# Kernel optimization log

Measured on AMD Instinct MI355X. Metric: run time of the kernel, lower is better.

The kernel has to match this reference:

```python
import jax, jax.numpy as jnp
import numpy as np

NUM_CLASSES = 22
H_IMG, W_IMG = 256, 320
VOTE_STEPS = 160          # number of discrete steps each pixel votes along its ray
VOTE_THRESH = 0.5         # inlier threshold used by HoughVoterPyTorch


def setup_inputs() -> dict:
    key = jax.random.key(0)
    ks = jax.random.split(key, 24)
    B = 4
    rn = lambda k, s, sc=1.0: (jax.random.normal(k, s, jnp.float32) * sc)
    inp = {
        'x1': rn(ks[0], (B, 512, 8, 10)),
        'x2': rn(ks[1], (B, 256, 16, 20)),
        'x3': rn(ks[2], (B, 128, 32, 40)),
        'x4': rn(ks[3], (B, 64, 64, 80)),
        'x5': rn(ks[4], (B, 64, 128, 160)),
        'depth': jax.random.uniform(ks[5], (B, 1, H_IMG, W_IMG), jnp.float32, 0.5, 3.0),
    }
    raw = jax.random.uniform(ks[6], (B, NUM_CLASSES, H_IMG, W_IMG), jnp.float32)
    inp['seg'] = jnp.where(raw > 0.97, raw, 0.0)  # sparse per-class responses
    inp['fx'] = jnp.float32(572.4); inp['fy'] = jnp.float32(573.6)
    inp['px'] = jnp.float32(W_IMG / 2); inp['py'] = jnp.float32(H_IMG / 2)
    # ConvTranspose2d weights in torch layout [Cin, Cout, kH, kW]
    inp['w5'] = rn(ks[7], (512, 256, 4, 4), 0.02); inp['b5'] = jnp.zeros((256,), jnp.float32)
    inp['w4'] = rn(ks[8], (512, 128, 4, 4), 0.02); inp['b4'] = jnp.zeros((128,), jnp.float32)
    inp['w3'] = rn(ks[9], (256, 64, 4, 4), 0.03);  inp['b3'] = jnp.zeros((64,), jnp.float32)
    inp['w2'] = rn(ks[10], (128, 64, 4, 4), 0.04); inp['b2'] = jnp.zeros((64,), jnp.float32)
    inp['w1'] = rn(ks[11], (128, 64, 4, 4), 0.04); inp['b1'] = jnp.zeros((64,), jnp.float32)
    inp['wv'] = rn(ks[12], (3 * NUM_CLASSES, 64), 0.1); inp['bv'] = jnp.zeros((3 * NUM_CLASSES,), jnp.float32)
    inp['wc'] = rn(ks[13], (NUM_CLASSES, 64), 0.1);     inp['bc'] = jnp.zeros((NUM_CLASSES,), jnp.float32)
    return inp


def conv_t(x, w, b):
    # torch ConvTranspose2d(k=4, s=2, p=1) == dilated conv with flipped kernel
    k = jnp.flip(w, (2, 3)).transpose(1, 0, 2, 3)  # [Cout, Cin, 4, 4]
    y = jax.lax.conv_general_dilated(x, k, (1, 1), ((2, 2), (2, 2)),
                                     lhs_dilation=(2, 2),
                                     dimension_numbers=('NCHW', 'OIHW', 'NCHW'))
    return y + b[None, :, None, None]


def hough_vote(seg2d, dirs, depth2d, fx, fy, px, py):
    # seg2d: [H,W] fused fg prob; dirs: [H,W,2] (dx,dy); depth2d: [H,W]
    H, W = seg2d.shape
    n = dirs / (jnp.linalg.norm(dirs, axis=-1, keepdims=True) + 1e-6)
    u = n[..., 0].reshape(-1)
    v = n[..., 1].reshape(-1)
    ys, xs = jnp.meshgrid(jnp.arange(H, dtype=jnp.float32),
                          jnp.arange(W, dtype=jnp.float32), indexing='ij')
    xs = xs.reshape(-1); ys = ys.reshape(-1)
    w = (seg2d * (seg2d > VOTE_THRESH)).reshape(-1)  # weighted fg votes

    def step(acc, t):
        xt = jnp.round(xs + t * u).astype(jnp.int32)
        yt = jnp.round(ys + t * v).astype(jnp.int32)
        inb = (xt >= 0) & (xt < W) & (yt >= 0) & (yt < H)
        idx = jnp.clip(yt, 0, H - 1) * W + jnp.clip(xt, 0, W - 1)
        return acc.at[idx].add(jnp.where(inb, w, 0.0)), None

    acc, _ = jax.lax.scan(step, jnp.zeros(H * W, jnp.float32),
                          jnp.arange(1, VOTE_STEPS + 1, dtype=jnp.float32))
    vote_map = acc.reshape(H, W)
    ci = jnp.argmax(acc)
    cy = (ci // W).astype(jnp.float32)
    cx = (ci % W).astype(jnp.float32)
    mask = (seg2d > VOTE_THRESH).astype(jnp.float32)
    tz = jnp.sum(depth2d * mask) / (jnp.sum(mask) + 1e-6)
    tx = (cx - px) * tz / fx
    ty = (cy - py) * tz / fy
    return vote_map, jnp.stack([cx, cy]), jnp.stack([tx, ty, tz])


def reference(x1, x2, x3, x4, x5, depth, seg, fx, fy, px, py,
              w5, b5, w4, b4, w3, b3, w2, b2, w1, b1, wv, bv, wc, bc):
    x = jax.nn.relu(conv_t(x1, w5, b5))
    x = jax.nn.relu(conv_t(jnp.concatenate([x, x2], 1), w4, b4))
    x = jax.nn.relu(conv_t(jnp.concatenate([x, x3], 1), w3, b3))
    x = jax.nn.relu(conv_t(jnp.concatenate([x, x4], 1), w2, b2))
    x = jax.nn.relu(conv_t(jnp.concatenate([x, x5], 1), w1, b1))
    bottom_vertex = jnp.einsum('bchw,oc->bohw', x, wv) + bv[None, :, None, None]
    logits = jnp.einsum('bchw,oc->bohw', x, wc) + bc[None, :, None, None]
    bottom_label = jnp.argmax(logits, axis=1)
    center_dirs = jnp.transpose(bottom_vertex[:, :2], (0, 2, 3, 1))  # [B,H,W,2]
    seg_fused = jnp.clip(jnp.sum(seg, axis=1), 0.0, 1.0)             # [B,H,W]
    vote_maps, centers, translations = jax.vmap(
        hough_vote, in_axes=(0, 0, 0, None, None, None, None)
    )(seg_fused, center_dirs, depth[:, 0], fx, fy, px, py)
    return bottom_vertex, bottom_label, vote_maps, centers, translations
```

## Files before the change

kernel.cpp:

```cpp
#include <hip/hip_runtime.h>
#include <cstdint>
#include <cstddef>

#define H_IMG 256
#define W_IMG 320
#define HW_IMG (H_IMG * W_IMG)
#define NCLS 22
#define VOTE_STEPS 160
#define TW 64
#define TH 64
#define NTX 5
#define NTY 4
#define NTILE (NTX * NTY)
#define NCHUNK 16
#define CHPIX (HW_IMG / NCHUNK)

__global__ void repack_kernel(const float* __restrict__ w, double* __restrict__ wp,
                              int CIN, int COUT) {
    int total = CIN * COUT * 16;
    for (int i = blockIdx.x * blockDim.x + threadIdx.x; i < total;
         i += gridDim.x * blockDim.x) {
        int j = i & 3;
        int co = (i >> 2) % COUT;
        int rest = (i >> 2) / COUT;
        int cin = rest % CIN;
        int pp = rest / CIN;
        int ry = pp >> 1, rx = pp & 1;
        int dy = j >> 1, dx = j & 1;
        int ky = 3 - ry - 2 * dy;
        int kx = 3 - rx - 2 * dx;
        wp[i] = (double)w[((size_t)cin * COUT + co) * 16 + ky * 4 + kx];
    }
}

__global__ void repackR_kernel(const float* __restrict__ w, double* __restrict__ wr,
                               int CIN, int COUT) {
    int NCOG = COUT >> 4;
    int total = CIN * COUT * 16;
    for (int i = blockIdx.x * blockDim.x + threadIdx.x; i < total;
         i += gridDim.x * blockDim.x) {
        int tap = i & 3;
        int co = (i >> 2) & 15;
        int rest = i >> 6;
        int cin = rest % CIN;
        int pc = rest / CIN;
        int cog = pc % NCOG;
        int pp = pc / NCOG;
        int ry = pp >> 1, rx = pp & 1;
        int dy = tap >> 1, dxx = tap & 1;
        int ky = 3 - ry - 2 * dy;
        int kx = 3 - rx - 2 * dxx;
        wr[i] = (double)w[((size_t)cin * COUT + (cog * 16 + co)) * 16 + ky * 4 + kx];
    }
}

__global__ void transpose_d_kernel(const float* __restrict__ w, double* __restrict__ wt,
                                   int O, int K) {
    int i = blockIdx.x * blockDim.x + threadIdx.x;
    if (i < O * K) {
        int o = i / K, k = i - o * K;
        wt[k * O + o] = (double)w[i];
    }
}

template <bool RELU_A, bool ADBL>
__global__ __launch_bounds__(320) void convt_part_kernel(
    const void* __restrict__ inA_, int CA,
    const float* __restrict__ inB, int CB,
    const double* __restrict__ wp,
    double* __restrict__ parts,
    int COUT, int Hin, int Win, int nSplit, int B, int TOT) {
    const int NCO = 16;
    const int CIN = CA + CB;
    const int cog = blockIdx.y >> 2;
    const int pp = blockIdx.y & 3;
    const int ry = pp >> 1, rx = pp & 1;
    const int b = blockIdx.z % B;
    const int sp = blockIdx.z / B;
    const int cinPer = CIN / nSplit;
    const int c0 = sp * cinPer, c1 = c0 + cinPer;
    const int co0 = cog * NCO;
    const int plane = Hin * Win;
    const int Hout = Hin * 2, Wout = Win * 2;
    const int bs = blockDim.x;
    double* out = parts + (size_t)sp * TOT;

    __shared__ double wl[64 * 64];
    for (int i = threadIdx.x; i < cinPer * 64; i += bs) {
        int ci = i >> 6, k = i & 63;
        wl[i] = wp[(((size_t)pp * CIN + c0 + ci) * COUT + co0) * 4 + k];
    }
    __syncthreads();

    for (int p = blockIdx.x * bs + threadIdx.x; p < plane; p += gridDim.x * bs) {
        int m = p / Win, n = p - m * Win;
        int iy0 = m + ry - 1, ix0 = n + rx - 1;
        int oy = 2 * m + ry, ox = 2 * n + rx;
        double f00 = (iy0 >= 0 && ix0 >= 0) ? 1.0 : 0.0;
        double f01 = (iy0 >= 0 && ix0 + 1 < Win) ? 1.0 : 0.0;
        double f10 = (iy0 + 1 < Hin && ix0 >= 0) ? 1.0 : 0.0;
        double f11 = (iy0 + 1 < Hin && ix0 + 1 < Win) ? 1.0 : 0.0;
        int cy0 = max(iy0, 0), cy1 = min(iy0 + 1, Hin - 1);
        int cx0 = max(ix0, 0), cx1 = min(ix0 + 1, Win - 1);
        int o00 = cy0 * Win + cx0, o01 = cy0 * Win + cx1;
        int o10 = cy1 * Win + cx0, o11 = cy1 * Win + cx1;

        double acc[16];
#pragma unroll
        for (int k = 0; k < 16; ++k) acc[k] = 0.0;

        int a0 = min(c0, CA), a1 = min(c1, CA);
        for (int c = a0; c < a1; ++c) {
            double x00, x01, x10, x11;
            if (ADBL) {
                const double* s = (const double*)inA_ + ((size_t)b * CA + c) * plane;
                x00 = f00 * s[o00]; x01 = f01 * s[o01];
                x10 = f10 * s[o10]; x11 = f11 * s[o11];
            } else {
                const float* s = (const float*)inA_ + ((size_t)b * CA + c) * plane;
                x00 = f00 * (double)s[o00]; x01 = f01 * (double)s[o01];
                x10 = f10 * (double)s[o10]; x11 = f11 * (double)s[o11];
            }
            if (RELU_A) {
                x00 = fmax(x00, 0.0); x01 = fmax(x01, 0.0);
                x10 = fmax(x10, 0.0); x11 = fmax(x11, 0.0);
            }
            const double2* w2 = (const double2*)&wl[(c - c0) * 64];
#pragma unroll
            for (int k = 0; k < 16; ++k) {
                double2 wa = w2[k * 2], wb = w2[k * 2 + 1];
                acc[k] += x00 * wa.x + x01 * wa.y + x10 * wb.x + x11 * wb.y;
            }
        }
        if (CB > 0 && c1 > CA) {
            int b0 = max(c0, CA) - CA, b1 = c1 - CA;
            const float* srcB = inB + (size_t)b * CB * plane;
            for (int c = b0; c < b1; ++c) {
                const float* s = srcB + (size_t)c * plane;
                double x00 = f00 * (double)s[o00], x01 = f01 * (double)s[o01];
                double x10 = f10 * (double)s[o10], x11 = f11 * (double)s[o11];
                const double2* w2 = (const double2*)&wl[(c + CA - c0) * 64];
#pragma unroll
                for (int k = 0; k < 16; ++k) {
                    double2 wa = w2[k * 2], wb = w2[k * 2 + 1];
                    acc[k] += x00 * wa.x + x01 * wa.y + x10 * wb.x + x11 * wb.y;
                }
            }
        }

        size_t ob = ((size_t)b * COUT + co0) * (size_t)Hout * Wout +
                    (size_t)oy * Wout + ox;
#pragma unroll
        for (int k = 0; k < 16; ++k)
            out[ob + (size_t)k * Hout * Wout] = acc[k];
    }
}

__global__ __launch_bounds__(320) void convt_part_l1_kernel(
    const float* __restrict__ xin, int CIN,
    const double* __restrict__ wp,
    double* __restrict__ parts,
    int COUT, int nSplit, int B, int TOT) {
    const int Hin = 8, Win = 10, plane = 80;
    const int Hout = 16, Wout = 20;
    const int cog = blockIdx.y;
    const int b = blockIdx.z % B;
    const int sp = blockIdx.z / B;
    const int cinPer = CIN / nSplit;
    const int c0 = sp * cinPer;
    const int co0 = cog * 16;
    const int pp = threadIdx.x / plane;
    const int p = threadIdx.x - pp * plane;
    const int ry = pp >> 1, rx = pp & 1;
    double* out = parts + (size_t)sp * TOT;

    __shared__ double wl[4 * 32 * 64];
    for (int i = threadIdx.x; i < 4 * cinPer * 64; i += 320) {
        int k = i & 63;
        int ci = (i >> 6) % cinPer;
        int pq = (i >> 6) / cinPer;
        wl[i] = wp[(((size_t)pq * CIN + c0 + ci) * COUT + co0) * 4 + k];
    }
    __syncthreads();

    int m = p / Win, n = p - m * Win;
    int iy0 = m + ry - 1, ix0 = n + rx - 1;
    int oy = 2 * m + ry, ox = 2 * n + rx;
    double f00 = (iy0 >= 0 && ix0 >= 0) ? 1.0 : 0.0;
    double f01 = (iy0 >= 0 && ix0 + 1 < Win) ? 1.0 : 0.0;
    double f10 = (iy0 + 1 < Hin && ix0 >= 0) ? 1.0 : 0.0;
    double f11 = (iy0 + 1 < Hin && ix0 + 1 < Win) ? 1.0 : 0.0;
    int cy0 = max(iy0, 0), cy1 = min(iy0 + 1, Hin - 1);
    int cx0 = max(ix0, 0), cx1 = min(ix0 + 1, Win - 1);
    int o00 = cy0 * Win + cx0, o01 = cy0 * Win + cx1;
    int o10 = cy1 * Win + cx0, o11 = cy1 * Win + cx1;

    double acc[16];
#pragma unroll
    for (int k = 0; k < 16; ++k) acc[k] = 0.0;

    const float* s = xin + ((size_t)b * CIN + c0) * plane;
    const double* wpp = &wl[pp * cinPer * 64];
    for (int c = 0; c < cinPer; ++c) {
        double x00 = f00 * (double)s[o00], x01 = f01 * (double)s[o01];
        double x10 = f10 * (double)s[o10], x11 = f11 * (double)s[o11];
        const double2* w2 = (const double2*)&wpp[c * 64];
#pragma unroll
        for (int k = 0; k < 16; ++k) {
            double2 wa = w2[k * 2], wb = w2[k * 2 + 1];
            acc[k] += x00 * wa.x + x01 * wa.y + x10 * wb.x + x11 * wb.y;
        }
        s += plane;
    }

    size_t ob = ((size_t)b * COUT + co0) * (size_t)Hout * Wout +
                (size_t)oy * Wout + ox;
#pragma unroll
    for (int k = 0; k < 16; ++k)
        out[ob + (size_t)k * Hout * Wout] = acc[k];
}

__global__ void reduce_part_kernel(const double* __restrict__ parts,
                                   const float* __restrict__ bias,
                                   double* __restrict__ out,
                                   int nSplit, int COUT, int HWo, int TOT) {
    int i = blockIdx.x * blockDim.x + threadIdx.x;
    if (i < TOT) {
        double a = (double)bias[(i / HWo) % COUT];
        for (int sp = 0; sp < nSplit; ++sp) a += parts[(size_t)sp * TOT + i];
        out[i] = a;
    }
}

template <int PX>
__global__ __launch_bounds__(256) void convt_reg_kernel(
    const double* __restrict__ zin, const float* __restrict__ xin,
    const double* __restrict__ wr,
    const float* __restrict__ bias,
    double* __restrict__ out,
    int COUT, int Hin, int Win) {
    const int NCOG = COUT >> 4;
    const int plane = Hin * Win;
    const int Wq = Win / PX;
    const int cog = blockIdx.y >> 2, pp = blockIdx.y & 3;
    const int ry = pp >> 1, rx = pp & 1;
    const int b = blockIdx.z;
    __shared__ double wl[4096];

    int t = blockIdx.x * 256 + threadIdx.x;
    int m = t / Wq, n0 = (t - m * Wq) * PX;
    int r0 = m + ry - 1, r1 = r0 + 1;
    double mr0 = (r0 >= 0) ? 1.0 : 0.0;
    double mr1 = (r1 < Hin) ? 1.0 : 0.0;
    int cr0 = max(r0, 0) * Win, cr1 = min(r1, Hin - 1) * Win;
    const int ib = rx ? 0 : 1;
    const int eidx = rx ? PX : 0;
    int eoff = rx ? min(n0 + PX, Win - 1) : max(n0 - 1, 0);
    double me = rx ? ((n0 + PX < Win) ? 1.0 : 0.0) : ((n0 > 0) ? 1.0 : 0.0);
    double me0 = me * mr0, me1 = me * mr1;

    double acc[16][PX];
#pragma unroll
    for (int k = 0; k < 16; ++k) {
        double bvv = (double)bias[cog * 16 + k];
#pragma unroll
        for (int tt = 0; tt < PX; ++tt) acc[k][tt] = bvv;
    }

    const double* wbase = wr + (size_t)(pp * NCOG + cog) * 128 * 64;

    for (int i = threadIdx.x; i < 4096; i += 256) wl[i] = wbase[i];
    __syncthreads();
    {
        const double* s = zin + (size_t)b * 64 * plane;
        for (int c = 0; c < 64; ++c) {
            double xa0[PX + 1], xa1[PX + 1];
#pragma unroll
            for (int j = 0; j < PX / 2; ++j) {
                double2 v0 = *(const double2*)(s + cr0 + n0 + 2 * j);
                double2 v1 = *(const double2*)(s + cr1 + n0 + 2 * j);
                xa0[ib + 2 * j] = mr0 * fmax(v0.x, 0.0);
                xa0[ib + 2 * j + 1] = mr0 * fmax(v0.y, 0.0);
                xa1[ib + 2 * j] = mr1 * fmax(v1.x, 0.0);
                xa1[ib + 2 * j + 1] = mr1 * fmax(v1.y, 0.0);
            }
            xa0[eidx] = me0 * fmax(s[cr0 + eoff], 0.0);
            xa1[eidx] = me1 * fmax(s[cr1 + eoff], 0.0);
            const double2* w2 = (const double2*)&wl[c * 64];
#pragma unroll
            for (int co = 0; co < 16; ++co) {
                double2 wa = w2[co * 2], wb = w2[co * 2 + 1];
#pragma unroll
                for (int tt = 0; tt < PX; ++tt)
                    acc[co][tt] += wa.x * xa0[tt] + wa.y * xa0[tt + 1] +
                                   wb.x * xa1[tt] + wb.y * xa1[tt + 1];
            }
            s += plane;
        }
    }
    __syncthreads();
    for (int i = threadIdx.x; i < 4096; i += 256) wl[i] = wbase[4096 + i];
    __syncthreads();
    {
        const float* s = xin + (size_t)b * 64 * plane;
        for (int c = 0; c < 64; ++c) {
            double xa0[PX + 1], xa1[PX + 1];
#pragma unroll
            for (int j = 0; j < PX / 2; ++j) {
                float2 v0 = *(const float2*)(s + cr0 + n0 + 2 * j);
                float2 v1 = *(const float2*)(s + cr1 + n0 + 2 * j);
                xa0[ib + 2 * j] = mr0 * (double)v0.x;
                xa0[ib + 2 * j + 1] = mr0 * (double)v0.y;
                xa1[ib + 2 * j] = mr1 * (double)v1.x;
                xa1[ib + 2 * j + 1] = mr1 * (double)v1.y;
            }
            xa0[eidx] = me0 * (double)s[cr0 + eoff];
            xa1[eidx] = me1 * (double)s[cr1 + eoff];
            const double2* w2 = (const double2*)&wl[c * 64];
#pragma unroll
            for (int co = 0; co < 16; ++co) {
                double2 wa = w2[co * 2], wb = w2[co * 2 + 1];
#pragma unroll
                for (int tt = 0; tt < PX; ++tt)
                    acc[co][tt] += wa.x * xa0[tt] + wa.y * xa0[tt + 1] +
                                   wb.x * xa1[tt] + wb.y * xa1[tt + 1];
            }
            s += plane;
        }
    }

    int oy = 2 * m + ry;
    size_t ob = (size_t)(b * COUT + cog * 16) * plane * 4 + (size_t)oy * (Win * 2);
#pragma unroll
    for (int co = 0; co < 16; ++co)
#pragma unroll
        for (int tt = 0; tt < PX; ++tt)
            out[ob + (size_t)co * plane * 4 + 2 * (n0 + tt) + rx] = acc[co][tt];
}

__global__ __launch_bounds__(256) void head_lds_kernel(
    const double* __restrict__ z5,
    const double* __restrict__ wvT,
    const float* __restrict__ bv,
    const double* __restrict__ wcT,
    const float* __restrict__ bc,
    float* __restrict__ vert, double* __restrict__ dirs,
    float* __restrict__ label) {
    int p = blockIdx.x * 256 + threadIdx.x;
    int half = blockIdx.y;
    int b = blockIdx.z;
    __shared__ double wl[64 * 44];
    if (half == 0) {
        for (int i = threadIdx.x; i < 64 * 44; i += 256) {
            int c = i / 44, k = i - c * 44;
            wl[i] = wvT[c * 66 + k];
        }
    } else {
        for (int i = threadIdx.x; i < 64 * 44; i += 256) {
            int c = i / 44, k = i - c * 44;
            wl[i] = (k < 22) ? wvT[c * 66 + 44 + k] : wcT[c * 22 + (k - 22)];
        }
    }
    __syncthreads();

    const double* xp = z5 + (size_t)b * 64 * HW_IMG + p;
    if (half == 0) {
        double acc[44];
#pragma unroll
        for (int k = 0; k < 44; ++k) acc[k] = (double)bv[k];
        for (int c = 0; c < 64; ++c) {
            double x = fmax(xp[(size_t)c * HW_IMG], 0.0);
            const double2* w2 = (const double2*)&wl[c * 44];
#pragma unroll
            for (int j = 0; j < 22; ++j) {
                double2 w = w2[j];
                acc[2 * j] += x * w.x; acc[2 * j + 1] += x * w.y;
            }
        }
        float* op = vert + (size_t)b * 66 * HW_IMG + p;
#pragma unroll
        for (int k = 0; k < 44; ++k) op[(size_t)k * HW_IMG] = (float)acc[k];
        dirs[(size_t)b * 2 * HW_IMG + p] = acc[0];
        dirs[(size_t)b * 2 * HW_IMG + HW_IMG + p] = acc[1];
    } else {
        double acc[22], lg[22];
#pragma unroll
        for (int k = 0; k < 22; ++k) { acc[k] = (double)bv[44 + k]; lg[k] = (double)bc[k]; }
        for (int c = 0; c < 64; ++c) {
            double x = fmax(xp[(size_t)c * HW_IMG], 0.0);
            const double2* w2 = (const double2*)&wl[c * 44];
#pragma unroll
            for (int j = 0; j < 11; ++j) {
                double2 w = w2[j];
                acc[2 * j] += x * w.x; acc[2 * j + 1] += x * w.y;
            }
#pragma unroll
            for (int j = 0; j < 11; ++j) {
                double2 w = w2[11 + j];
                lg[2 * j] += x * w.x; lg[2 * j + 1] += x * w.y;
            }
        }
        float* op = vert + ((size_t)b * 66 + 44) * HW_IMG + p;
#pragma unroll
        for (int k = 0; k < 22; ++k) op[(size_t)k * HW_IMG] = (float)acc[k];
        int bi = 0; double bvv = lg[0];
#pragma unroll
        for (int k = 1; k < 22; ++k)
            if (lg[k] > bvv) { bvv = lg[k]; bi = k; }
        label[(size_t)b * HW_IMG + p] = (float)bi;
    }
}

__global__ __launch_bounds__(256) void vote_prep_kernel(
    const float* __restrict__ seg, const float* __restrict__ depth,
    const double* __restrict__ dirs,
    double* __restrict__ rayS, double* __restrict__ rayU,
    double* __restrict__ rayV, double* __restrict__ rayRU,
    double* __restrict__ rayRV, double* __restrict__ rayN,
    double* __restrict__ sums) {
    int p = blockIdx.x * 256 + threadIdx.x;
    int b = blockIdx.z;
    double s = 0.0;
    const float* sp = seg + (size_t)b * NCLS * HW_IMG + p;
    for (int c = 0; c < NCLS; ++c) s += (double)sp[(size_t)c * HW_IMG];
    s = fmin(fmax(s, 0.0), 1.0);
    bool msk = s > 0.5;
    double d = (double)depth[(size_t)b * HW_IMG + p];
    double dm = msk ? d : 0.0;
    double mm = msk ? 1.0 : 0.0;
    for (int off = 32; off > 0; off >>= 1) {
        dm += __shfl_down(dm, off);
        mm += __shfl_down(mm, off);
    }
    __shared__ double sdm[4], smm[4];
    int wid = threadIdx.x >> 6, lane = threadIdx.x & 63;
    if (lane == 0) { sdm[wid] = dm; smm[wid] = mm; }
    __syncthreads();
    if (threadIdx.x == 0) {
        atomicAdd(&sums[b * 2 + 0], sdm[0] + sdm[1] + sdm[2] + sdm[3]);
        atomicAdd(&sums[b * 2 + 1], smm[0] + smm[1] + smm[2] + smm[3]);
    }
    size_t idx = (size_t)b * HW_IMG + p;
    if (msk) {
        double dx = dirs[(size_t)b * 2 * HW_IMG + p];
        double dy = dirs[(size_t)b * 2 * HW_IMG + HW_IMG + p];
        double nrm = sqrt(dx * dx + dy * dy) + 1e-6;
        double u = dx / nrm, v = dy / nrm;
        double xf = (double)(p % W_IMG), yf = (double)(p / W_IMG);
        double tmax = 1e30;
        if (u > 1e-9)       tmax = fmin(tmax, ((double)W_IMG - 0.25 - xf) / u);
        else if (u < -1e-9) tmax = fmin(tmax, (-0.75 - xf) / u);
        if (v > 1e-9)       tmax = fmin(tmax, ((double)H_IMG - 0.25 - yf) / v);
        else if (v < -1e-9) tmax = fmin(tmax, (-0.75 - yf) / v);
        int nst = VOTE_STEPS;
        if (tmax < (double)VOTE_STEPS) nst = (int)tmax + 1;
        rayS[idx] = s;
        rayU[idx] = u;
        rayV[idx] = v;
        rayRU[idx] = (u != 0.0) ? 1.0 / u : 0.0;
        rayRV[idx] = (v != 0.0) ? 1.0 / v : 0.0;
        rayN[idx] = (double)nst;
    } else {
        rayS[idx] = 0.0;
    }
}

__global__ __launch_bounds__(256) void vote_tile_kernel(
    const double* __restrict__ rayS, const double* __restrict__ rayU,
    const double* __restrict__ rayV, const double* __restrict__ rayRU,
    const double* __restrict__ rayRV, const double* __restrict__ rayN,
    double* __restrict__ vparts) {
    int chunk = blockIdx.x;
    int tile = blockIdx.y;
    int b = blockIdx.z;
    int tx0 = (tile % NTX) * TW, ty0 = (tile / NTX) * TH;
    __shared__ double vt[TW * TH];
    for (int i = threadIdx.x; i < TW * TH; i += 256) vt[i] = 0.0;
    __syncthreads();

    size_t base = (size_t)b * HW_IMG;
    int p0 = chunk * CHPIX;
    for (int q = threadIdx.x; q < CHPIX; q += 256) {
        int p = p0 + q;
        double s = rayS[base + p];
        if (s == 0.0) continue;
        double u = rayU[base + p], v = rayV[base + p];
        double ru = rayRU[base + p], rv = rayRV[base + p];
        int nst = (int)rayN[base + p];
        double xf = (double)(p % W_IMG), yf = (double)(p / W_IMG);
        double ta = 1.0, tb = (double)nst;
        if (ru != 0.0) {
            double lo = ((double)(tx0 - 1) - xf) * ru;
            double hi = ((double)(tx0 + TW) - xf) * ru;
            ta = fmax(ta, fmin(lo, hi));
            tb = fmin(tb, fmax(lo, hi));
        } else {
            if (xf < (double)(tx0 - 1) || xf > (double)(tx0 + TW)) continue;
        }
        if (rv != 0.0) {
            double lo = ((double)(ty0 - 1) - yf) * rv;
            double hi = ((double)(ty0 + TH) - yf) * rv;
            ta = fmax(ta, fmin(lo, hi));
            tb = fmin(tb, fmax(lo, hi));
        } else {
            if (yf < (double)(ty0 - 1) || yf > (double)(ty0 + TH)) continue;
        }
        if (ta > tb) continue;
        int t0 = (int)ceil(ta), t1 = (int)floor(tb);
        for (int t = t0; t <= t1; ++t) {
            double tf = (double)t;
            int xi = (int)rint(xf + tf * u);
            int yi = (int)rint(yf + tf * v);
            if (xi >= tx0 && xi < tx0 + TW && yi >= ty0 && yi < ty0 + TH)
                atomicAdd(&vt[(yi - ty0) * TW + (xi - tx0)], s);
        }
    }
    __syncthreads();
    double* dst = vparts + (((size_t)chunk * 4 + b) * NTILE + tile) * (TW * TH);
    for (int i = threadIdx.x; i < TW * TH; i += 256) dst[i] = vt[i];
}

__global__ void vote_reduce_kernel(const double* __restrict__ vparts,
                                   double* __restrict__ voteacc,
                                   float* __restrict__ vote) {
    int i = blockIdx.x * 256 + threadIdx.x;
    if (i < 4 * HW_IMG) {
        int b = i / HW_IMG, cell = i - b * HW_IMG;
        int y = cell / W_IMG, x = cell - y * W_IMG;
        int tile = (y / TH) * NTX + (x / TW);
        int ci = (y % TH) * TW + (x % TW);
        double a = 0.0;
        for (int c = 0; c < NCHUNK; ++c)
            a += vparts[(((size_t)c * 4 + b) * NTILE + tile) * (TW * TH) + ci];
        voteacc[i] = a;
        vote[i] = (float)a;
    }
}

__global__ __launch_bounds__(1024) void center_d_kernel(
    const double* __restrict__ voteacc, const double* __restrict__ sums,
    const float* __restrict__ fx, const float* __restrict__ fy,
    const float* __restrict__ px, const float* __restrict__ py,
    float* __restrict__ centers, float* __restrict__ transl) {
    int b = blockIdx.x;
    const double* vb = voteacc + (size_t)b * HW_IMG;
    double best = -1.0;
    int bi = HW_IMG;
    for (int i = threadIdx.x; i < HW_IMG; i += 1024) {
        double v = vb[i];
        if (v > best || (v == best && i < bi)) { best = v; bi = i; }
    }
    for (int off = 32; off > 0; off >>= 1) {
        double ov = __shfl_down(best, off);
        int oi = __shfl_down(bi, off);
        if (ov > best || (ov == best && oi < bi)) { best = ov; bi = oi; }
    }
    __shared__ double sbv[16];
    __shared__ int sbi[16];
    int wid = threadIdx.x >> 6, lane = threadIdx.x & 63;
    if (lane == 0) { sbv[wid] = best; sbi[wid] = bi; }
    __syncthreads();
    if (threadIdx.x == 0) {
        for (int q = 1; q < 16; ++q)
            if (sbv[q] > best || (sbv[q] == best && sbi[q] < bi)) {
                best = sbv[q]; bi = sbi[q];
            }
        double cx = (double)(bi % W_IMG), cy = (double)(bi / W_IMG);
        double tz = sums[b * 2 + 0] / (sums[b * 2 + 1] + 1e-6);
        double tx = (cx - (double)px[0]) * tz / (double)fx[0];
        double ty = (cy - (double)py[0]) * tz / (double)fy[0];
        centers[b * 2 + 0] = (float)cx;
        centers[b * 2 + 1] = (float)cy;
        transl[b * 3 + 0] = (float)tx;
        transl[b * 3 + 1] = (float)ty;
        transl[b * 3 + 2] = (float)tz;
    }
}

extern "C" void kernel_launch(void* const* d_in, const int* in_sizes, int n_in,
                              void* d_out, int out_size, void* d_ws, size_t ws_size,
                              hipStream_t stream) {
    const float* x1 = (const float*)d_in[0];
    const float* x2 = (const float*)d_in[1];
    const float* x3 = (const float*)d_in[2];
    const float* x4 = (const float*)d_in[3];
    const float* x5 = (const float*)d_in[4];
    const float* depth = (const float*)d_in[5];
    const float* seg = (const float*)d_in[6];
    const float* fx = (const float*)d_in[7];
    const float* fy = (const float*)d_in[8];
    const float* px = (const float*)d_in[9];
    const float* py = (const float*)d_in[10];
    const float* w5 = (const float*)d_in[11];
    const float* b5 = (const float*)d_in[12];
    const float* w4 = (const float*)d_in[13];
    const float* b4 = (const float*)d_in[14];
    const float* w3 = (const float*)d_in[15];
    const float* b3 = (const float*)d_in[16];
    const float* w2 = (const float*)d_in[17];
    const float* b2 = (const float*)d_in[18];
    const float* w1 = (const float*)d_in[19];
    const float* b1 = (const float*)d_in[20];
    const float* wv = (const float*)d_in[21];
    const float* bv = (const float*)d_in[22];
    const float* wc = (const float*)d_in[23];
    const float* bc = (const float*)d_in[24];

    float* out = (float*)d_out;
    float* vert = out;
    float* label = vert + (size_t)4 * 66 * HW_IMG;
    float* vote = label + (size_t)4 * HW_IMG;
    float* centers = vote + (size_t)4 * HW_IMG;
    float* transl = centers + 8;

    double* zA = (double*)d_ws;
    double* zB = zA + 20971520;
    double* dirs = zB + 5242880;
    double* voteacc = dirs + 655360;
    double* sums = voteacc + 327680;
    double* wp5 = sums + 8;
    double* wp4 = wp5 + 2097152;
    double* wp3 = wp4 + 1048576;
    double* wr2 = wp3 + 262144;
    double* wr1 = wr2 + 131072;
    double* wvT = wr1 + 131072;
    double* wcT = wvT + 4224;
    double* z1 = zA; double* z2 = zB; double* z3 = zA; double* z4 = zB; double* z5 = zA;
    double* parts = zA + 2000000;
    double* rayS = zB;
    double* rayU = zB + 327680;
    double* rayV = zB + 2 * 327680;
    double* rayRU = zB + 3 * 327680;
    double* rayRV = zB + 4 * 327680;
    double* rayN = zB + 5 * 327680;
    double* vparts = zA;

    hipMemsetAsync(sums, 0, 8 * sizeof(double), stream);

    auto rp = [&](const float* w, double* wp, int CIN, int COUT) {
        int total = CIN * COUT * 16;
        repack_kernel<<<(total + 255) / 256, 256, 0, stream>>>(w, wp, CIN, COUT);
    };
    rp(w5, wp5, 512, 256);
    rp(w4, wp4, 512, 128);
    rp(w3, wp3, 256, 64);
    repackR_kernel<<<(131072 + 255) / 256, 256, 0, stream>>>(w2, wr2, 128, 64);
    repackR_kernel<<<(131072 + 255) / 256, 256, 0, stream>>>(w1, wr1, 128, 64);
    transpose_d_kernel<<<(66 * 64 + 255) / 256, 256, 0, stream>>>(wv, wvT, 66, 64);
    transpose_d_kernel<<<(22 * 64 + 255) / 256, 256, 0, stream>>>(wc, wcT, 22, 64);

    convt_part_l1_kernel<<<dim3(1, 16, 64), 320, 0, stream>>>(
        x1, 512, wp5, parts, 256, 16, 4, 327680);
    reduce_part_kernel<<<1280, 256, 0, stream>>>(parts, b5, z1, 16, 256, 320, 327680);
    convt_part_kernel<true, true><<<dim3(1, 32, 32), 320, 0, stream>>>(
        z1, 256, x2, 256, wp4, parts, 128, 16, 20, 8, 4, 655360);
    reduce_part_kernel<<<2560, 256, 0, stream>>>(parts, b4, z2, 8, 128, 1280, 655360);
    convt_part_kernel<true, true><<<dim3(5, 16, 16), 256, 0, stream>>>(
        z2, 128, x3, 128, wp3, parts, 64, 32, 40, 4, 4, 1310720);
    reduce_part_kernel<<<5120, 256, 0, stream>>>(parts, b3, z3, 4, 64, 5120, 1310720);
    convt_reg_kernel<2><<<dim3(10, 16, 4), 256, 0, stream>>>(
        z3, x4, wr2, b2, z4, 64, 64, 80);
    convt_reg_kernel<2><<<dim3(40, 16, 4), 256, 0, stream>>>(
        z4, x5, wr1, b1, z5, 64, 128, 160);

    head_lds_kernel<<<dim3(320, 2, 4), 256, 0, stream>>>(z5, wvT, bv, wcT, bc,
                                                         vert, dirs, label);

    vote_prep_kernel<<<dim3(320, 1, 4), 256, 0, stream>>>(
        seg, depth, dirs, rayS, rayU, rayV, rayRU, rayRV, rayN, sums);
    vote_tile_kernel<<<dim3(NCHUNK, NTILE, 4), 256, 0, stream>>>(
        rayS, rayU, rayV, rayRU, rayRV, rayN, vparts);
    vote_reduce_kernel<<<(4 * HW_IMG + 255) / 256, 256, 0, stream>>>(
        vparts, voteacc, vote);
    center_d_kernel<<<4, 1024, 0, stream>>>(voteacc, sums, fx, fy, px, py,
                                            centers, transl);
}
```

Baseline: 1.955 ms.

## Merge weight prep launches, split conv layer by input half, fuse vote prep into head

All seven weight repack and transpose kernels become one grid-stride kernel, cutting launch count. The per-pixel vote preparation (seg sum, masked depth reduction, ray setup) moves into the head kernel's first half, so the separate pass and the intermediate dirs buffer go away. The fourth transposed conv is split across its two input sources (z3 and x4) into twice as many blocks, with an extra elementwise add-in pass. That adds parallelism but costs a full read-modify-write of a large double buffer.

```diff
diff --git a/kernel.cpp b/kernel.cpp
--- a/kernel.cpp
+++ b/kernel.cpp
@@ -15,51 +15,65 @@
 #define NCHUNK 16
 #define CHPIX (HW_IMG / NCHUNK)
 
-__global__ void repack_kernel(const float* __restrict__ w, double* __restrict__ wp,
-                              int CIN, int COUT) {
-    int total = CIN * COUT * 16;
-    for (int i = blockIdx.x * blockDim.x + threadIdx.x; i < total;
-         i += gridDim.x * blockDim.x) {
-        int j = i & 3;
-        int co = (i >> 2) % COUT;
-        int rest = (i >> 2) / COUT;
-        int cin = rest % CIN;
-        int pp = rest / CIN;
-        int ry = pp >> 1, rx = pp & 1;
-        int dy = j >> 1, dx = j & 1;
-        int ky = 3 - ry - 2 * dy;
-        int kx = 3 - rx - 2 * dx;
-        wp[i] = (double)w[((size_t)cin * COUT + co) * 16 + ky * 4 + kx];
-    }
-}
-
-__global__ void repackR_kernel(const float* __restrict__ w, double* __restrict__ wr,
-                               int CIN, int COUT) {
+__device__ inline double repack_elem(const float* __restrict__ w,
+                                     int CIN, int COUT, int i) {
+    int j = i & 3;
+    int co = (i >> 2) % COUT;
+    int rest = (i >> 2) / COUT;
+    int cin = rest % CIN;
+    int pp = rest / CIN;
+    int ry = pp >> 1, rx = pp & 1;
+    int dy = j >> 1, dx = j & 1;
+    int ky = 3 - ry - 2 * dy;
+    int kx = 3 - rx - 2 * dx;
+    return (double)w[((size_t)cin * COUT + co) * 16 + ky * 4 + kx];
+}
+
+__device__ inline double repackR_elem(const float* __restrict__ w,
+                                      int CIN, int COUT, int i) {
     int NCOG = COUT >> 4;
-    int total = CIN * COUT * 16;
-    for (int i = blockIdx.x * blockDim.x + threadIdx.x; i < total;
-         i += gridDim.x * blockDim.x) {
-        int tap = i & 3;
-        int co = (i >> 2) & 15;
-        int rest = i >> 6;
-        int cin = rest % CIN;
-        int pc = rest / CIN;
-        int cog = pc % NCOG;
-        int pp = pc / NCOG;
-        int ry = pp >> 1, rx = pp & 1;
-        int dy = tap >> 1, dxx = tap & 1;
-        int ky = 3 - ry - 2 * dy;
-        int kx = 3 - rx - 2 * dxx;
-        wr[i] = (double)w[((size_t)cin * COUT + (cog * 16 + co)) * 16 + ky * 4 + kx];
-    }
-}
-
-__global__ void transpose_d_kernel(const float* __restrict__ w, double* __restrict__ wt,
-                                   int O, int K) {
-    int i = blockIdx.x * blockDim.x + threadIdx.x;
-    if (i < O * K) {
-        int o = i / K, k = i - o * K;
-        wt[k * O + o] = (double)w[i];
+    int tap = i & 3;
+    int co = (i >> 2) & 15;
+    int rest = i >> 6;
+    int cin = rest % CIN;
+    int pc = rest / CIN;
+    int cog = pc % NCOG;
+    int pp = pc / NCOG;
+    int ry = pp >> 1, rx = pp & 1;
+    int dy = tap >> 1, dxx = tap & 1;
+    int ky = 3 - ry - 2 * dy;
+    int kx = 3 - rx - 2 * dxx;
+    return (double)w[((size_t)cin * COUT + (cog * 16 + co)) * 16 + ky * 4 + kx];
+}
+
+__global__ void prep_weights_kernel(
+    const float* __restrict__ w5, const float* __restrict__ w4,
+    const float* __restrict__ w3, const float* __restrict__ w2,
+    const float* __restrict__ w1, const float* __restrict__ wv,
+    const float* __restrict__ wc,
+    double* __restrict__ wp5, double* __restrict__ wp4,
+    double* __restrict__ wp3, double* __restrict__ wr2,
+    double* __restrict__ wr1, double* __restrict__ wvT,
+    double* __restrict__ wcT) {
+    const int S0 = 2097152, S1 = 1048576, S2 = 262144;
+    const int S3 = 131072, S4 = 131072, S5 = 4224, S6 = 1408;
+    const int total = S0 + S1 + S2 + S3 + S4 + S5 + S6;
+    for (int g = blockIdx.x * 256 + threadIdx.x; g < total;
+         g += gridDim.x * 256) {
+        int i = g;
+        if (i < S0) { wp5[i] = repack_elem(w5, 512, 256, i); continue; }
+        i -= S0;
+        if (i < S1) { wp4[i] = repack_elem(w4, 512, 128, i); continue; }
+        i -= S1;
+        if (i < S2) { wp3[i] = repack_elem(w3, 256, 64, i); continue; }
+        i -= S2;
+        if (i < S3) { wr2[i] = repackR_elem(w2, 128, 64, i); continue; }
+        i -= S3;
+        if (i < S4) { wr1[i] = repackR_elem(w1, 128, 64, i); continue; }
+        i -= S4;
+        if (i < S5) { int o = i / 64, k = i - o * 64; wvT[k * 66 + o] = (double)wv[i]; continue; }
+        i -= S5;
+        { int o = i / 64, k = i - o * 64; wcT[k * 22 + o] = (double)wc[i]; }
     }
 }
 
@@ -232,6 +246,12 @@
     }
 }
 
+__global__ void addin_kernel(double* __restrict__ out,
+                             const double* __restrict__ parts, int TOT) {
+    int i = blockIdx.x * blockDim.x + threadIdx.x;
+    if (i < TOT) out[i] += parts[i];
+}
+
 template <int PX>
 __global__ __launch_bounds__(256) void convt_reg_kernel(
     const double* __restrict__ zin, const float* __restrict__ xin,
@@ -338,14 +358,123 @@
             out[ob + (size_t)co * plane * 4 + 2 * (n0 + tt) + rx] = acc[co][tt];
 }
 
-__global__ __launch_bounds__(256) void head_lds_kernel(
+template <int PX>
+__global__ __launch_bounds__(256) void convt_reg_split_kernel(
+    const double* __restrict__ zin, const float* __restrict__ xin,
+    const double* __restrict__ wr,
+    const float* __restrict__ bias,
+    double* __restrict__ out, double* __restrict__ parts,
+    int COUT, int Hin, int Win, int B) {
+    const int NCOG = COUT >> 4;
+    const int plane = Hin * Win;
+    const int Wq = Win / PX;
+    const int cog = blockIdx.y >> 2, pp = blockIdx.y & 3;
+    const int ry = pp >> 1, rx = pp & 1;
+    const int b = blockIdx.z % B;
+    const int ch = blockIdx.z / B;
+    __shared__ double wl[4096];
+
+    int t = blockIdx.x * 256 + threadIdx.x;
+    int m = t / Wq, n0 = (t - m * Wq) * PX;
+    int r0 = m + ry - 1, r1 = r0 + 1;
+    double mr0 = (r0 >= 0) ? 1.0 : 0.0;
+    double mr1 = (r1 < Hin) ? 1.0 : 0.0;
+    int cr0 = max(r0, 0) * Win, cr1 = min(r1, Hin - 1) * Win;
+    const int ib = rx ? 0 : 1;
+    const int eidx = rx ? PX : 0;
+    int eoff = rx ? min(n0 + PX, Win - 1) : max(n0 - 1, 0);
+    double me = rx ? ((n0 + PX < Win) ? 1.0 : 0.0) : ((n0 > 0) ? 1.0 : 0.0);
+    double me0 = me * mr0, me1 = me * mr1;
+
+    double acc[16][PX];
+#pragma unroll
+    for (int k = 0; k < 16; ++k) {
+        double bvv = (ch == 1) ? (double)bias[cog * 16 + k] : 0.0;
+#pragma unroll
+        for (int tt = 0; tt < PX; ++tt) acc[k][tt] = bvv;
+    }
+
+    const double* wbase = wr + (size_t)(pp * NCOG + cog) * 128 * 64 +
+                          (size_t)ch * 4096;
+    for (int i = threadIdx.x; i < 4096; i += 256) wl[i] = wbase[i];
+    __syncthreads();
+
+    if (ch == 0) {
+        const double* s = zin + (size_t)b * 64 * plane;
+        for (int c = 0; c < 64; ++c) {
+            double xa0[PX + 1], xa1[PX + 1];
+#pragma unroll
+            for (int j = 0; j < PX / 2; ++j) {
+                double2 v0 = *(const double2*)(s + cr0 + n0 + 2 * j);
+                double2 v1 = *(const double2*)(s + cr1 + n0 + 2 * j);
+                xa0[ib + 2 * j] = mr0 * fmax(v0.x, 0.0);
+                xa0[ib + 2 * j + 1] = mr0 * fmax(v0.y, 0.0);
+                xa1[ib + 2 * j] = mr1 * fmax(v1.x, 0.0);
+                xa1[ib + 2 * j + 1] = mr1 * fmax(v1.y, 0.0);
+            }
+            xa0[eidx] = me0 * fmax(s[cr0 + eoff], 0.0);
+            xa1[eidx] = me1 * fmax(s[cr1 + eoff], 0.0);
+            const double2* w2 = (const double2*)&wl[c * 64];
+#pragma unroll
+            for (int co = 0; co < 16; ++co) {
+                double2 wa = w2[co * 2], wb = w2[co * 2 + 1];
+#pragma unroll
+                for (int tt = 0; tt < PX; ++tt)
+                    acc[co][tt] += wa.x * xa0[tt] + wa.y * xa0[tt + 1] +
+                                   wb.x * xa1[tt] + wb.y * xa1[tt + 1];
+            }
+            s += plane;
+        }
+    } else {
+        const float* s = xin + (size_t)b * 64 * plane;
+        for (int c = 0; c < 64; ++c) {
+            double xa0[PX + 1], xa1[PX + 1];
+#pragma unroll
+            for (int j = 0; j < PX / 2; ++j) {
+                float2 v0 = *(const float2*)(s + cr0 + n0 + 2 * j);
+                float2 v1 = *(const float2*)(s + cr1 + n0 + 2 * j);
+                xa0[ib + 2 * j] = mr0 * (double)v0.x;
+                xa0[ib + 2 * j + 1] = mr0 * (double)v0.y;
+                xa1[ib + 2 * j] = mr1 * (double)v1.x;
+                xa1[ib + 2 * j + 1] = mr1 * (double)v1.y;
+            }
+            xa0[eidx] = me0 * (double)s[cr0 + eoff];
+            xa1[eidx] = me1 * (double)s[cr1 + eoff];
+            const double2* w2 = (const double2*)&wl[c * 64];
+#pragma unroll
+            for (int co = 0; co < 16; ++co) {
+                double2 wa = w2[co * 2], wb = w2[co * 2 + 1];
+#pragma unroll
+                for (int tt = 0; tt < PX; ++tt)
+                    acc[co][tt] += wa.x * xa0[tt] + wa.y * xa0[tt + 1] +
+                                   wb.x * xa1[tt] + wb.y * xa1[tt + 1];
+            }
+            s += plane;
+        }
+    }
+
+    int oy = 2 * m + ry;
+    double* dst = (ch == 0) ? parts : out;
+    size_t ob = (size_t)(b * COUT + cog * 16) * plane * 4 + (size_t)oy * (Win * 2);
+#pragma unroll
+    for (int co = 0; co < 16; ++co)
+#pragma unroll
+        for (int tt = 0; tt < PX; ++tt)
+            dst[ob + (size_t)co * plane * 4 + 2 * (n0 + tt) + rx] = acc[co][tt];
+}
+
+__global__ __launch_bounds__(256) void head_vote_kernel(
     const double* __restrict__ z5,
     const double* __restrict__ wvT,
     const float* __restrict__ bv,
     const double* __restrict__ wcT,
     const float* __restrict__ bc,
-    float* __restrict__ vert, double* __restrict__ dirs,
-    float* __restrict__ label) {
+    const float* __restrict__ seg, const float* __restrict__ depth,
+    float* __restrict__ vert, float* __restrict__ label,
+    double* __restrict__ rayS, double* __restrict__ rayU,
+    double* __restrict__ rayV, double* __restrict__ rayRU,
+    double* __restrict__ rayRV, double* __restrict__ rayN,
+    double* __restrict__ sums) {
     int p = blockIdx.x * 256 + threadIdx.x;
     int half = blockIdx.y;
     int b = blockIdx.z;
@@ -365,6 +494,13 @@
 
     const double* xp = z5 + (size_t)b * 64 * HW_IMG + p;
     if (half == 0) {
+        double s_ = 0.0;
+        const float* sp = seg + (size_t)b * NCLS * HW_IMG + p;
+        for (int c = 0; c < NCLS; ++c) s_ += (double)sp[(size_t)c * HW_IMG];
+        s_ = fmin(fmax(s_, 0.0), 1.0);
+        bool msk = s_ > 0.5;
+        double d = (double)depth[(size_t)b * HW_IMG + p];
+
         double acc[44];
 #pragma unroll
         for (int k = 0; k < 44; ++k) acc[k] = (double)bv[k];
@@ -380,8 +516,44 @@
         float* op = vert + (size_t)b * 66 * HW_IMG + p;
 #pragma unroll
         for (int k = 0; k < 44; ++k) op[(size_t)k * HW_IMG] = (float)acc[k];
-        dirs[(size_t)b * 2 * HW_IMG + p] = acc[0];
-        dirs[(size_t)b * 2 * HW_IMG + HW_IMG + p] = acc[1];
+
+        double dm = msk ? d : 0.0;
+        double mm = msk ? 1.0 : 0.0;
+        for (int off = 32; off > 0; off >>= 1) {
+            dm += __shfl_down(dm, off);
+            mm += __shfl_down(mm, off);
+        }
+        __shared__ double sdm[4], smm[4];
+        int wid = threadIdx.x >> 6, lane = threadIdx.x & 63;
+        if (lane == 0) { sdm[wid] = dm; smm[wid] = mm; }
+        __syncthreads();
+        if (threadIdx.x == 0) {
+            atomicAdd(&sums[b * 2 + 0], sdm[0] + sdm[1] + sdm[2] + sdm[3]);
+            atomicAdd(&sums[b * 2 + 1], smm[0] + smm[1] + smm[2] + smm[3]);
+        }
+
+        size_t idx = (size_t)b * HW_IMG + p;
+        if (msk) {
+            double dx = acc[0], dy = acc[1];
+            double nrm = sqrt(dx * dx + dy * dy) + 1e-6;
+            double u = dx / nrm, v = dy / nrm;
+            double xf = (double)(p % W_IMG), yf = (double)(p / W_IMG);
+            double tmax = 1e30;
+            if (u > 1e-9)       tmax = fmin(tmax, ((double)W_IMG - 0.25 - xf) / u);
+            else if (u < -1e-9) tmax = fmin(tmax, (-0.75 - xf) / u);
+            if (v > 1e-9)       tmax = fmin(tmax, ((double)H_IMG - 0.25 - yf) / v);
+            else if (v < -1e-9) tmax = fmin(tmax, (-0.75 - yf) / v);
+            int nst = VOTE_STEPS;
+            if (tmax < (double)VOTE_STEPS) nst = (int)tmax + 1;
+            rayS[idx] = s_;
+            rayU[idx] = u;
+            rayV[idx] = v;
+            rayRU[idx] = (u != 0.0) ? 1.0 / u : 0.0;
+            rayRV[idx] = (v != 0.0) ? 1.0 / v : 0.0;
+            rayN[idx] = (double)nst;
+        } else {
+            rayS[idx] = 0.0;
+        }
     } else {
         double acc[22], lg[22];
 #pragma unroll
@@ -408,60 +580,6 @@
         for (int k = 1; k < 22; ++k)
             if (lg[k] > bvv) { bvv = lg[k]; bi = k; }
         label[(size_t)b * HW_IMG + p] = (float)bi;
-    }
-}
-
-__global__ __launch_bounds__(256) void vote_prep_kernel(
-    const float* __restrict__ seg, const float* __restrict__ depth,
-    const double* __restrict__ dirs,
-    double* __restrict__ rayS, double* __restrict__ rayU,
-    double* __restrict__ rayV, double* __restrict__ rayRU,
-    double* __restrict__ rayRV, double* __restrict__ rayN,
-    double* __restrict__ sums) {
-    int p = blockIdx.x * 256 + threadIdx.x;
-    int b = blockIdx.z;
-    double s = 0.0;
-    const float* sp = seg + (size_t)b * NCLS * HW_IMG + p;
-    for (int c = 0; c < NCLS; ++c) s += (double)sp[(size_t)c * HW_IMG];
-    s = fmin(fmax(s, 0.0), 1.0);
-    bool msk = s > 0.5;
-    double d = (double)depth[(size_t)b * HW_IMG + p];
-    double dm = msk ? d : 0.0;
-    double mm = msk ? 1.0 : 0.0;
-    for (int off = 32; off > 0; off >>= 1) {
-        dm += __shfl_down(dm, off);
-        mm += __shfl_down(mm, off);
-    }
-    __shared__ double sdm[4], smm[4];
-    int wid = threadIdx.x >> 6, lane = threadIdx.x & 63;
-    if (lane == 0) { sdm[wid] = dm; smm[wid] = mm; }
-    __syncthreads();
-    if (threadIdx.x == 0) {
-        atomicAdd(&sums[b * 2 + 0], sdm[0] + sdm[1] + sdm[2] + sdm[3]);
-        atomicAdd(&sums[b * 2 + 1], smm[0] + smm[1] + smm[2] + smm[3]);
-    }
-    size_t idx = (size_t)b * HW_IMG + p;
-    if (msk) {
-        double dx = dirs[(size_t)b * 2 * HW_IMG + p];
-        double dy = dirs[(size_t)b * 2 * HW_IMG + HW_IMG + p];
-        double nrm = sqrt(dx * dx + dy * dy) + 1e-6;
-        double u = dx / nrm, v = dy / nrm;
-        double xf = (double)(p % W_IMG), yf = (double)(p / W_IMG);
-        double tmax = 1e30;
-        if (u > 1e-9)       tmax = fmin(tmax, ((double)W_IMG - 0.25 - xf) / u);
-        else if (u < -1e-9) tmax = fmin(tmax, (-0.75 - xf) / u);
-        if (v > 1e-9)       tmax = fmin(tmax, ((double)H_IMG - 0.25 - yf) / v);
-        else if (v < -1e-9) tmax = fmin(tmax, (-0.75 - yf) / v);
-        int nst = VOTE_STEPS;
-        if (tmax < (double)VOTE_STEPS) nst = (int)tmax + 1;
-        rayS[idx] = s;
-        rayU[idx] = u;
-        rayV[idx] = v;
-        rayRU[idx] = (u != 0.0) ? 1.0 / u : 0.0;
-        rayRV[idx] = (v != 0.0) ? 1.0 / v : 0.0;
-        rayN[idx] = (double)nst;
-    } else {
-        rayS[idx] = 0.0;
     }
 }
 
@@ -615,8 +733,8 @@
 
     double* zA = (double*)d_ws;
     double* zB = zA + 20971520;
-    double* dirs = zB + 5242880;
-    double* voteacc = dirs + 655360;
+    double* dirs_unused = zB + 5242880;
+    double* voteacc = dirs_unused + 655360;
     double* sums = voteacc + 327680;
     double* wp5 = sums + 8;
     double* wp4 = wp5 + 2097152;
@@ -637,17 +755,8 @@
 
     hipMemsetAsync(sums, 0, 8 * sizeof(double), stream);
 
-    auto rp = [&](const float* w, double* wp, int CIN, int COUT) {
-        int total = CIN * COUT * 16;
-        repack_kernel<<<(total + 255) / 256, 256, 0, stream>>>(w, wp, CIN, COUT);
-    };
-    rp(w5, wp5, 512, 256);
-    rp(w4, wp4, 512, 128);
-    rp(w3, wp3, 256, 64);
-    repackR_kernel<<<(131072 + 255) / 256, 256, 0, stream>>>(w2, wr2, 128, 64);
-    repackR_kernel<<<(131072 + 255) / 256, 256, 0, stream>>>(w1, wr1, 128, 64);
-    transpose_d_kernel<<<(66 * 64 + 255) / 256, 256, 0, stream>>>(wv, wvT, 66, 64);
-    transpose_d_kernel<<<(22 * 64 + 255) / 256, 256, 0, stream>>>(wc, wcT, 22, 64);
+    prep_weights_kernel<<<2048, 256, 0, stream>>>(
+        w5, w4, w3, w2, w1, wv, wc, wp5, wp4, wp3, wr2, wr1, wvT, wcT);
 
     convt_part_l1_kernel<<<dim3(1, 16, 64), 320, 0, stream>>>(
         x1, 512, wp5, parts, 256, 16, 4, 327680);
@@ -658,16 +767,16 @@
     convt_part_kernel<true, true><<<dim3(5, 16, 16), 256, 0, stream>>>(
         z2, 128, x3, 128, wp3, parts, 64, 32, 40, 4, 4, 1310720);
     reduce_part_kernel<<<5120, 256, 0, stream>>>(parts, b3, z3, 4, 64, 5120, 1310720);
-    convt_reg_kernel<2><<<dim3(10, 16, 4), 256, 0, stream>>>(
-        z3, x4, wr2, b2, z4, 64, 64, 80);
+    convt_reg_split_kernel<2><<<dim3(10, 16, 8), 256, 0, stream>>>(
+        z3, x4, wr2, b2, z4, parts, 64, 64, 80, 4);
+    addin_kernel<<<(5242880 + 255) / 256, 256, 0, stream>>>(z4, parts, 5242880);
     convt_reg_kernel<2><<<dim3(40, 16, 4), 256, 0, stream>>>(
         z4, x5, wr1, b1, z5, 64, 128, 160);
 
-    head_lds_kernel<<<dim3(320, 2, 4), 256, 0, stream>>>(z5, wvT, bv, wcT, bc,
-                                                         vert, dirs, label);
-
-    vote_prep_kernel<<<dim3(320, 1, 4), 256, 0, stream>>>(
-        seg, depth, dirs, rayS, rayU, rayV, rayRU, rayRV, rayN, sums);
+    head_vote_kernel<<<dim3(320, 2, 4), 256, 0, stream>>>(
+        z5, wvT, bv, wcT, bc, seg, depth, vert, label,
+        rayS, rayU, rayV, rayRU, rayRV, rayN, sums);
+
     vote_tile_kernel<<<dim3(NCHUNK, NTILE, 4), 256, 0, stream>>>(
         rayS, rayU, rayV, rayRU, rayRV, rayN, vparts);
     vote_reduce_kernel<<<(4 * HW_IMG + 255) / 256, 256, 0, stream>>>(
```

New measurement: 1.957 ms. About the same (+0.1%).
